# Kernel optimization log

Hardware: AMD Instinct MI355X
Metric: run time of the kernel (lower is better)

## Reference

```python
import jax, jax.numpy as jnp
import numpy as np

B, S, H, DFF, HD = 2, 8192, 1024, 4096, 128


def setup_inputs() -> dict:
    key = jax.random.key(0)
    ks = jax.random.split(key, 10)
    hidden_states = jax.random.normal(ks[0], (B, S, H), jnp.float32)
    labels = jax.random.randint(ks[1], (B, S), 0, 32000)
    labels = jnp.where(jax.random.uniform(ks[2], (B, S)) < 0.1, -100, labels).astype(jnp.int64)
    cos = jax.random.normal(ks[3], (B, S, HD), jnp.float32)
    sin = jax.random.normal(ks[4], (B, S, HD), jnp.float32)
    cu_seq_lens_q = (jnp.arange(B + 1) * S).astype(jnp.int32)
    # gate params: random (instead of the degenerate all-keep init) so the mask varies
    Wg = jax.random.normal(ks[5], (H, 1), jnp.float32) * 0.05
    bg = jnp.zeros((1,), jnp.float32)
    # wrapped layer instantiated as a token-wise FFN: relu(x W1 + b1) W2 + b2
    W1 = jax.random.normal(ks[6], (H, DFF), jnp.float32) * 0.02
    b1 = jnp.zeros((DFF,), jnp.float32)
    W2 = jax.random.normal(ks[7], (DFF, H), jnp.float32) * 0.02
    b2 = jnp.zeros((H,), jnp.float32)
    return {"hidden_states": hidden_states, "cos": cos, "sin": sin,
            "Wg": Wg, "bg": bg, "W1": W1, "b1": b1, "W2": W2, "b2": b2,
            "labels": labels, "cu_seq_lens_q": cu_seq_lens_q}


def reference(hidden_states, cos, sin, Wg, bg, W1, b1, W2, b2, labels, cu_seq_lens_q):
    # per-token gate in fp32: sigmoid(Linear(h -> 1))
    logits = hidden_states.astype(jnp.float32) @ Wg + bg          # [B,S,1]
    w = jax.nn.sigmoid(logits).astype(hidden_states.dtype)         # [B,S,1]
    # keep mask: gate >= 0.5, force-keep ignored-label tokens
    mask = (w[..., 0] >= 0.5) | (labels == -100)                   # [B,S]
    # scale kept tokens by the gate weight before the wrapped layer
    xg = hidden_states * w                                         # [B,S,H]
    # token-wise wrapped layer (FFN): gather->layer->scatter == mask * layer(xg)
    y = jax.nn.relu(xg @ W1 + b1) @ W2 + b2                        # [B,S,H]
    # dropped tokens produce exact zeros in the output (scatter into zeros_like)
    out = jnp.where(mask[..., None], y, jnp.zeros_like(y))
    return out
```

## Files before the change

kernel.cpp:

```cpp
#include <hip/hip_runtime.h>
#include <hip/hip_bf16.h>


#define TOK 16384
#define HID 1024
#define FF  4096

typedef __attribute__((ext_vector_type(8))) __bf16 bf16x8;
typedef __attribute__((ext_vector_type(4))) float f32x4;

__device__ __forceinline__ void gload_lds16(const void* g, void* l) {
  __builtin_amdgcn_global_load_lds((const __attribute__((address_space(1))) void*)g,
                                   (__attribute__((address_space(3))) void*)l, 16, 0, 0);
}

__global__ __launch_bounds__(256) void k_transpose(const float* __restrict__ src,
                                                   __hip_bfloat16* __restrict__ dst,
                                                   int R, int C) {
  __shared__ float tile[32][33];
  const int c0 = blockIdx.x * 32, r0 = blockIdx.y * 32;
  const int tx = threadIdx.x, ty = threadIdx.y;
#pragma unroll
  for (int i = 0; i < 32; i += 8)
    tile[ty + i][tx] = src[(size_t)(r0 + ty + i) * C + (c0 + tx)];
  __syncthreads();
#pragma unroll
  for (int i = 0; i < 32; i += 8)
    dst[(size_t)(c0 + ty + i) * R + (r0 + tx)] = __float2bfloat16(tile[tx][ty + i]);
}

__global__ __launch_bounds__(256) void k_gate(const float* __restrict__ h,
                                              const float* __restrict__ wg,
                                              const float* __restrict__ bgp,
                                              const int* __restrict__ labels,
                                              float* __restrict__ out,
                                              __hip_bfloat16* __restrict__ A,
                                              int* __restrict__ idx,
                                              int* __restrict__ cnt) {
  const int t = blockIdx.x;
  const int tid = threadIdx.x;
  const float4 hv = ((const float4*)(h + (size_t)t * HID))[tid];
  const float4 gv = ((const float4*)wg)[tid];
  float d = hv.x * gv.x + hv.y * gv.y + hv.z * gv.z + hv.w * gv.w;
#pragma unroll
  for (int o = 32; o > 0; o >>= 1) d += __shfl_down(d, o, 64);
  __shared__ float ps[4];
  __shared__ int mrow;
  if ((tid & 63) == 0) ps[tid >> 6] = d;
  __syncthreads();
  const float logit = ps[0] + ps[1] + ps[2] + ps[3] + bgp[0];
  const bool keep = (logit >= 0.0f) || (labels[t] == -100);
  if (keep) {
    if (tid == 0) { int m = atomicAdd(cnt, 1); idx[m] = t; mrow = m; }
    __syncthreads();
    const int m = mrow;
    const float w = 1.0f / (1.0f + __expf(-logit));
    union { ushort4 u; __hip_bfloat16 b[4]; } pk;
    pk.b[0] = __float2bfloat16(hv.x * w);
    pk.b[1] = __float2bfloat16(hv.y * w);
    pk.b[2] = __float2bfloat16(hv.z * w);
    pk.b[3] = __float2bfloat16(hv.w * w);
    ((ushort4*)(A + (size_t)m * HID))[tid] = pk.u;
  } else {
    ((float4*)(out + (size_t)t * HID))[tid] = make_float4(0.f, 0.f, 0.f, 0.f);
  }
}


__global__ __launch_bounds__(256, 2) void k_gemm1(const __hip_bfloat16* __restrict__ A,
                                                  const __hip_bfloat16* __restrict__ Bt,
                                                  const float* __restrict__ bias,
                                                  __hip_bfloat16* __restrict__ Act,
                                                  const int* __restrict__ cnt) {
  const int Mc = *cnt;
  const int m0 = blockIdx.x * 128;
  if (m0 >= Mc) return;
  const int n0 = blockIdx.y * 128;

  __shared__ __hip_bfloat16 lA[128 * 64];
  __shared__ __hip_bfloat16 lB[128 * 64];

  const int tid = threadIdx.x;
  const int wave = tid >> 6, lane = tid & 63;
  const int wr = (wave >> 1) * 64, wc = (wave & 1) * 64;
  const int fm = lane & 15, quad = lane >> 4;

  const int srow = (lane >> 3);
  const int sg   = ((lane & 7) ^ srow) * 8;

  f32x4 acc[4][4] = {};

  const __hip_bfloat16* gA = A  + (size_t)(m0 + wave * 32 + srow) * HID + sg;
  const __hip_bfloat16* gB = Bt + (size_t)(n0 + wave * 32 + srow) * HID + sg;
  char* dA = (char*)lA + wave * 4096;
  char* dB = (char*)lB + wave * 4096;

  for (int kt = 0; kt < HID; kt += 64) {
    __syncthreads();
#pragma unroll
    for (int c = 0; c < 4; ++c) {
      gload_lds16(gA + (size_t)(c * 8) * HID + kt, dA + c * 1024);
      gload_lds16(gB + (size_t)(c * 8) * HID + kt, dB + c * 1024);
    }
    __syncthreads();
#pragma unroll
    for (int ks = 0; ks < 2; ++ks) {
      bf16x8 af[4], bb[4];
#pragma unroll
      for (int i = 0; i < 4; ++i)
        af[i] = *(const bf16x8*)&lA[(wr + i * 16 + fm) * 64 + (((ks * 4 + quad) ^ (fm & 7)) * 8)];
#pragma unroll
      for (int j = 0; j < 4; ++j)
        bb[j] = *(const bf16x8*)&lB[(wc + j * 16 + fm) * 64 + (((ks * 4 + quad) ^ (fm & 7)) * 8)];
#pragma unroll
      for (int i = 0; i < 4; ++i)
#pragma unroll
        for (int j = 0; j < 4; ++j)
          acc[i][j] = __builtin_amdgcn_mfma_f32_16x16x32_bf16(af[i], bb[j], acc[i][j], 0, 0, 0);
    }
  }

#pragma unroll
  for (int j = 0; j < 4; ++j) {
    const int col = n0 + wc + j * 16 + fm;
    const float bv = bias[col];
#pragma unroll
    for (int i = 0; i < 4; ++i) {
      const int rbase = m0 + wr + i * 16 + quad * 4;
#pragma unroll
      for (int r = 0; r < 4; ++r) {
        float v = acc[i][j][r] + bv;
        v = v > 0.f ? v : 0.f;
        Act[(size_t)(rbase + r) * FF + col] = __float2bfloat16(v);
      }
    }
  }
}

__global__ __launch_bounds__(256, 2) void k_gemm2(const __hip_bfloat16* __restrict__ Act,
                                                  const __hip_bfloat16* __restrict__ Bt,
                                                  const float* __restrict__ bias,
                                                  const int* __restrict__ idx,
                                                  float* __restrict__ out,
                                                  const int* __restrict__ cnt) {
  const int Mc = *cnt;
  const int m0 = blockIdx.x * 128;
  if (m0 >= Mc) return;
  const int n0 = blockIdx.y * 128;

  __shared__ __hip_bfloat16 lA[128 * 64];
  __shared__ __hip_bfloat16 lB[128 * 64];

  const int tid = threadIdx.x;
  const int wave = tid >> 6, lane = tid & 63;
  const int wr = (wave >> 1) * 64, wc = (wave & 1) * 64;
  const int fm = lane & 15, quad = lane >> 4;
  const int srow = (lane >> 3);
  const int sg   = ((lane & 7) ^ srow) * 8;

  f32x4 acc[4][4] = {};

  const __hip_bfloat16* gA = Act + (size_t)(m0 + wave * 32 + srow) * FF + sg;
  const __hip_bfloat16* gB = Bt  + (size_t)(n0 + wave * 32 + srow) * FF + sg;
  char* dA = (char*)lA + wave * 4096;
  char* dB = (char*)lB + wave * 4096;

  for (int kt = 0; kt < FF; kt += 64) {
    __syncthreads();
#pragma unroll
    for (int c = 0; c < 4; ++c) {
      gload_lds16(gA + (size_t)(c * 8) * FF + kt, dA + c * 1024);
      gload_lds16(gB + (size_t)(c * 8) * FF + kt, dB + c * 1024);
    }
    __syncthreads();
#pragma unroll
    for (int ks = 0; ks < 2; ++ks) {
      bf16x8 af[4], bb[4];
#pragma unroll
      for (int i = 0; i < 4; ++i)
        af[i] = *(const bf16x8*)&lA[(wr + i * 16 + fm) * 64 + (((ks * 4 + quad) ^ (fm & 7)) * 8)];
#pragma unroll
      for (int j = 0; j < 4; ++j)
        bb[j] = *(const bf16x8*)&lB[(wc + j * 16 + fm) * 64 + (((ks * 4 + quad) ^ (fm & 7)) * 8)];
#pragma unroll
      for (int i = 0; i < 4; ++i)
#pragma unroll
        for (int j = 0; j < 4; ++j)
          acc[i][j] = __builtin_amdgcn_mfma_f32_16x16x32_bf16(af[i], bb[j], acc[i][j], 0, 0, 0);
    }
  }

#pragma unroll
  for (int i = 0; i < 4; ++i) {
#pragma unroll
    for (int r = 0; r < 4; ++r) {
      const int m = m0 + wr + i * 16 + quad * 4 + r;
      if (m < Mc) {
        const int t = idx[m];
        float* orow = out + (size_t)t * HID + n0 + wc + fm;
#pragma unroll
        for (int j = 0; j < 4; ++j)
          orow[j * 16] = acc[i][j][r] + bias[n0 + wc + j * 16 + fm];
      }
    }
  }
}

extern "C" void kernel_launch(void* const* d_in, const int* in_sizes, int n_in,
                              void* d_out, int out_size, void* d_ws, size_t ws_size,
                              hipStream_t stream) {
  const float* h   = (const float*)d_in[0];
  const float* Wg  = (const float*)d_in[3];
  const float* bg  = (const float*)d_in[4];
  const float* W1  = (const float*)d_in[5];
  const float* b1  = (const float*)d_in[6];
  const float* W2  = (const float*)d_in[7];
  const float* b2  = (const float*)d_in[8];
  const int*  labels = (const int*)d_in[9];
  float* out = (float*)d_out;

  char* ws = (char*)d_ws;
  int* cnt            = (int*)(ws + 0);
  int* idx            = (int*)(ws + 1024);
  __hip_bfloat16* W1t = (__hip_bfloat16*)(ws + (1u  << 17));
  __hip_bfloat16* W2t = (__hip_bfloat16*)(ws + (16u << 20));
  __hip_bfloat16* A   = (__hip_bfloat16*)(ws + (32u << 20));
  __hip_bfloat16* Act = (__hip_bfloat16*)(ws + (64ull << 20));

  hipMemsetAsync(cnt, 0, 4, stream);
  k_transpose<<<dim3(FF / 32, HID / 32), dim3(32, 8), 0, stream>>>(W1, W1t, HID, FF);
  k_transpose<<<dim3(HID / 32, FF / 32), dim3(32, 8), 0, stream>>>(W2, W2t, FF, HID);
  k_gate<<<TOK, 256, 0, stream>>>(h, Wg, bg, labels, out, A, idx, cnt);
  k_gemm1<<<dim3(TOK / 128, FF / 128), 256, 0, stream>>>(A, W1t, b1, Act, cnt);
  k_gemm2<<<dim3(TOK / 128, HID / 128), 256, 0, stream>>>(Act, W2t, b2, idx, out, cnt);
}
```

Baseline: 439.7 us.

## Double-buffer LDS in second GEMM and batch gate over 16 tokens per block

The second GEMM now uses two LDS buffers, so the global-to-LDS load for the next K tile is issued before computing the current one, with one barrier per iteration instead of two. The gate kernel handles 16 tokens per block, one wave per token row, and does a single atomicAdd per block to reserve compacted slots, cutting atomic contention and block count. The costs are double the LDS in gemm2, which may lower occupancy, and a second read of each kept hidden row in the gate kernel.

```diff
diff --git a/kernel.cpp b/kernel.cpp
--- a/kernel.cpp
+++ b/kernel.cpp
@@ -29,6 +29,7 @@
     dst[(size_t)(c0 + ty + i) * R + (r0 + tx)] = __float2bfloat16(tile[tx][ty + i]);
 }
 
+#define GTOK 16
 __global__ __launch_bounds__(256) void k_gate(const float* __restrict__ h,
                                               const float* __restrict__ wg,
                                               const float* __restrict__ bgp,
@@ -37,32 +38,75 @@
                                               __hip_bfloat16* __restrict__ A,
                                               int* __restrict__ idx,
                                               int* __restrict__ cnt) {
-  const int t = blockIdx.x;
   const int tid = threadIdx.x;
-  const float4 hv = ((const float4*)(h + (size_t)t * HID))[tid];
-  const float4 gv = ((const float4*)wg)[tid];
-  float d = hv.x * gv.x + hv.y * gv.y + hv.z * gv.z + hv.w * gv.w;
-#pragma unroll
-  for (int o = 32; o > 0; o >>= 1) d += __shfl_down(d, o, 64);
-  __shared__ float ps[4];
-  __shared__ int mrow;
-  if ((tid & 63) == 0) ps[tid >> 6] = d;
-  __syncthreads();
-  const float logit = ps[0] + ps[1] + ps[2] + ps[3] + bgp[0];
-  const bool keep = (logit >= 0.0f) || (labels[t] == -100);
-  if (keep) {
-    if (tid == 0) { int m = atomicAdd(cnt, 1); idx[m] = t; mrow = m; }
-    __syncthreads();
-    const int m = mrow;
-    const float w = 1.0f / (1.0f + __expf(-logit));
-    union { ushort4 u; __hip_bfloat16 b[4]; } pk;
-    pk.b[0] = __float2bfloat16(hv.x * w);
-    pk.b[1] = __float2bfloat16(hv.y * w);
-    pk.b[2] = __float2bfloat16(hv.z * w);
-    pk.b[3] = __float2bfloat16(hv.w * w);
-    ((ushort4*)(A + (size_t)m * HID))[tid] = pk.u;
-  } else {
-    ((float4*)(out + (size_t)t * HID))[tid] = make_float4(0.f, 0.f, 0.f, 0.f);
+  const int wave = tid >> 6, lane = tid & 63;
+  const int t0 = blockIdx.x * GTOK;
+
+  float4 gv[4];
+#pragma unroll
+  for (int it = 0; it < 4; ++it) gv[it] = ((const float4*)wg)[it * 64 + lane];
+
+  __shared__ float slogit[GTOK];
+  __shared__ int sslot[GTOK];
+
+#pragma unroll
+  for (int r = 0; r < 4; ++r) {
+    const int li = r * 4 + wave;
+    const float* hrow = h + (size_t)(t0 + li) * HID;
+    float d = 0.f;
+#pragma unroll
+    for (int it = 0; it < 4; ++it) {
+      const float4 hv = ((const float4*)hrow)[it * 64 + lane];
+      d += hv.x * gv[it].x + hv.y * gv[it].y + hv.z * gv[it].z + hv.w * gv[it].w;
+    }
+#pragma unroll
+    for (int o = 32; o > 0; o >>= 1) d += __shfl_down(d, o, 64);
+    if (lane == 0) slogit[li] = d;
+  }
+  __syncthreads();
+
+  if (tid == 0) {
+    const float bg = bgp[0];
+    int slots[GTOK];
+    int n = 0;
+#pragma unroll
+    for (int li = 0; li < GTOK; ++li) {
+      const bool keep = (slogit[li] + bg >= 0.0f) || (labels[t0 + li] == -100);
+      slots[li] = keep ? n++ : -1;
+    }
+    const int base = atomicAdd(cnt, n);
+#pragma unroll
+    for (int li = 0; li < GTOK; ++li)
+      sslot[li] = slots[li] >= 0 ? base + slots[li] : -1;
+  }
+  __syncthreads();
+
+#pragma unroll
+  for (int r = 0; r < 4; ++r) {
+    const int li = r * 4 + wave;
+    const int t = t0 + li;
+    const int m = sslot[li];
+    const float* hrow = h + (size_t)t * HID;
+    if (m >= 0) {
+      if (lane == 0) idx[m] = t;
+      const float logit = slogit[li] + bgp[0];
+      const float w = 1.0f / (1.0f + __expf(-logit));
+#pragma unroll
+      for (int it = 0; it < 4; ++it) {
+        const float4 hv = ((const float4*)hrow)[it * 64 + lane];
+        union { ushort4 u; __hip_bfloat16 b[4]; } pk;
+        pk.b[0] = __float2bfloat16(hv.x * w);
+        pk.b[1] = __float2bfloat16(hv.y * w);
+        pk.b[2] = __float2bfloat16(hv.z * w);
+        pk.b[3] = __float2bfloat16(hv.w * w);
+        ((ushort4*)(A + (size_t)m * HID))[it * 64 + lane] = pk.u;
+      }
+    } else {
+      const float4 z = make_float4(0.f, 0.f, 0.f, 0.f);
+#pragma unroll
+      for (int it = 0; it < 4; ++it)
+        ((float4*)(out + (size_t)t * HID))[it * 64 + lane] = z;
+    }
   }
 }
 
@@ -148,8 +192,8 @@
   if (m0 >= Mc) return;
   const int n0 = blockIdx.y * 128;
 
-  __shared__ __hip_bfloat16 lA[128 * 64];
-  __shared__ __hip_bfloat16 lB[128 * 64];
+  __shared__ __hip_bfloat16 lA[2][128 * 64];
+  __shared__ __hip_bfloat16 lB[2][128 * 64];
 
   const int tid = threadIdx.x;
   const int wave = tid >> 6, lane = tid & 63;
@@ -162,33 +206,46 @@
 
   const __hip_bfloat16* gA = Act + (size_t)(m0 + wave * 32 + srow) * FF + sg;
   const __hip_bfloat16* gB = Bt  + (size_t)(n0 + wave * 32 + srow) * FF + sg;
-  char* dA = (char*)lA + wave * 4096;
-  char* dB = (char*)lB + wave * 4096;
-
-  for (int kt = 0; kt < FF; kt += 64) {
-    __syncthreads();
+
+  auto stage = [&](int b, int kt) {
+    char* dA = (char*)lA[b] + wave * 4096;
+    char* dB = (char*)lB[b] + wave * 4096;
 #pragma unroll
     for (int c = 0; c < 4; ++c) {
       gload_lds16(gA + (size_t)(c * 8) * FF + kt, dA + c * 1024);
       gload_lds16(gB + (size_t)(c * 8) * FF + kt, dB + c * 1024);
     }
-    __syncthreads();
+  };
+  auto compute = [&](int b) {
+    const __hip_bfloat16* sA = lA[b];
+    const __hip_bfloat16* sB = lB[b];
 #pragma unroll
     for (int ks = 0; ks < 2; ++ks) {
       bf16x8 af[4], bb[4];
 #pragma unroll
       for (int i = 0; i < 4; ++i)
-        af[i] = *(const bf16x8*)&lA[(wr + i * 16 + fm) * 64 + (((ks * 4 + quad) ^ (fm & 7)) * 8)];
+        af[i] = *(const bf16x8*)&sA[(wr + i * 16 + fm) * 64 + (((ks * 4 + quad) ^ (fm & 7)) * 8)];
 #pragma unroll
       for (int j = 0; j < 4; ++j)
-        bb[j] = *(const bf16x8*)&lB[(wc + j * 16 + fm) * 64 + (((ks * 4 + quad) ^ (fm & 7)) * 8)];
+        bb[j] = *(const bf16x8*)&sB[(wc + j * 16 + fm) * 64 + (((ks * 4 + quad) ^ (fm & 7)) * 8)];
 #pragma unroll
       for (int i = 0; i < 4; ++i)
 #pragma unroll
         for (int j = 0; j < 4; ++j)
           acc[i][j] = __builtin_amdgcn_mfma_f32_16x16x32_bf16(af[i], bb[j], acc[i][j], 0, 0, 0);
     }
-  }
+  };
+
+  stage(0, 0);
+  __syncthreads();
+  int cur = 0;
+  for (int kt = 64; kt < FF; kt += 64) {
+    stage(cur ^ 1, kt);
+    compute(cur);
+    __syncthreads();
+    cur ^= 1;
+  }
+  compute(cur);
 
 #pragma unroll
   for (int i = 0; i < 4; ++i) {
@@ -230,7 +287,7 @@
   hipMemsetAsync(cnt, 0, 4, stream);
   k_transpose<<<dim3(FF / 32, HID / 32), dim3(32, 8), 0, stream>>>(W1, W1t, HID, FF);
   k_transpose<<<dim3(HID / 32, FF / 32), dim3(32, 8), 0, stream>>>(W2, W2t, FF, HID);
-  k_gate<<<TOK, 256, 0, stream>>>(h, Wg, bg, labels, out, A, idx, cnt);
+  k_gate<<<TOK / GTOK, 256, 0, stream>>>(h, Wg, bg, labels, out, A, idx, cnt);
   k_gemm1<<<dim3(TOK / 128, FF / 128), 256, 0, stream>>>(A, W1t, b1, Act, cnt);
   k_gemm2<<<dim3(TOK / 128, HID / 128), 256, 0, stream>>>(Act, W2t, b2, idx, out, cnt);
 }
```

Result: faster. 393.1 us (-10.6%).
